# Kernel optimization log

Hardware: AMD Instinct MI355X
Metric: run time of the kernel (lower is better)

Reference implementation:

```python
import jax, jax.numpy as jnp
import numpy as np

N, C, P, K = 100000, 64, 64, 16  # points, in_planes, planes, nsample
EPS = 1e-5

def _bn(y, g, b, m, v):
    # inference-mode batchnorm over channel (last) dim
    return (y - m) * (g * jax.lax.rsqrt(v + EPS)) + b

def setup_inputs() -> dict:
    key = jax.random.key(0)
    ks = jax.random.split(key, 12)
    p = jax.random.normal(ks[0], (N, 3), jnp.float32)
    x = jax.random.normal(ks[1], (N, C), jnp.float32)
    idx = jax.random.randint(ks[2], (N, K), 0, N, jnp.int32)
    s = 0.05
    w1 = jax.random.normal(ks[3], (C, P), jnp.float32) * s
    conv_w = jax.random.normal(ks[4], (P, P + 3), jnp.float32) * s  # Conv1d(P+3, P, 1) weight squeezed
    w3 = jax.random.normal(ks[5], (P, P), jnp.float32) * s
    def bn_params(k):
        k1, k2 = jax.random.split(k)
        return (jnp.ones((P,), jnp.float32),                      # gamma
                jnp.zeros((P,), jnp.float32),                     # beta
                jax.random.normal(k1, (P,), jnp.float32) * 0.01,  # running mean
                jnp.abs(jax.random.normal(k2, (P,), jnp.float32)) * 0.1 + 1.0)  # running var
    g1, b1, m1, v1 = bn_params(ks[6])
    g2, b2, m2, v2 = bn_params(ks[7])
    g3, b3, m3, v3 = bn_params(ks[8])
    return dict(p=p, x=x, idx=idx, w1=w1, g1=g1, b1=b1, m1=m1, v1=v1,
                conv_w=conv_w, g2=g2, b2=b2, m2=m2, v2=v2,
                w3=w3, g3=g3, b3=b3, m3=m3, v3=v3)

def reference(p, x, idx, w1, g1, b1, m1, v1, conv_w, g2, b2, m2, v2, w3, g3, b3, m3, v3):
    identity = x
    h = jax.nn.relu(_bn(x @ w1, g1, b1, m1, v1))                     # [N, P]
    # queryandgroup with use_xyz=True: concat(relative xyz, neighbor feats)
    rel = p[idx] - p[:, None, :]                                      # [N, K, 3]
    grouped = jnp.concatenate([rel, h[idx]], axis=-1)                 # [N, K, 3+P]
    e = jnp.einsum('nkc,oc->nko', grouped, conv_w)                    # conv1x1 -> [N, K, P]
    e = jax.nn.relu(_bn(e, g2, b2, m2, v2))
    f = jnp.max(e, axis=1)                                            # max over neighbors -> [N, P]
    out = jax.nn.relu(_bn(f @ w3, g3, b3, m3, v3) + identity)         # [N, P]
    return out
```

## Files before the change

kernel.cpp:

```cpp
#include <hip/hip_runtime.h>
#include <stdint.h>


#define EPS 1e-5f

typedef unsigned short u16;
typedef unsigned int u32;
typedef __attribute__((ext_vector_type(8))) short bf16x8;
typedef __attribute__((ext_vector_type(4))) float f32x4;

__device__ __forceinline__ float b2f(u16 u) { return __uint_as_float(((u32)u) << 16); }
__device__ __forceinline__ u16 f2b(float f) {
    u32 u = __float_as_uint(f);
    u32 r = u + 0x7fffu + ((u >> 16) & 1u);
    return (u16)(r >> 16);
}
__device__ __forceinline__ bool is_bf16(const void* g) { return ((const u32*)g)[0] == 0x3F803F80u; }
__device__ __forceinline__ float ldval(const void* p, size_t i, bool isbf) {
    return isbf ? b2f(((const u16*)p)[i]) : ((const float*)p)[i];
}
#define MFMA16(a, b, c) __builtin_amdgcn_mfma_f32_16x16x32_bf16(a, b, c, 0, 0, 0)

__device__ __forceinline__ bf16x8 asbf(uint4 u) {
    union { uint4 u; bf16x8 b; } c;
    c.u = u;
    return c.b;
}

__device__ __forceinline__ bf16x8 ldrow8(const void* base, size_t row, int coff, bool isbf) {
    if (isbf) {
        const u16* pp = (const u16*)base + row * 64 + coff;
        return asbf(*(const uint4*)pp);
    } else {
        const float* pp = (const float*)base + row * 64 + coff;
        float4 q0 = ((const float4*)pp)[0], q1 = ((const float4*)pp)[1];
        bf16x8 r;
        r[0] = (short)f2b(q0.x); r[1] = (short)f2b(q0.y);
        r[2] = (short)f2b(q0.z); r[3] = (short)f2b(q0.w);
        r[4] = (short)f2b(q1.x); r[5] = (short)f2b(q1.y);
        r[6] = (short)f2b(q1.z); r[7] = (short)f2b(q1.w);
        return r;
    }
}

__global__ void __launch_bounds__(256)
k_prep(const void* __restrict__ w1, const void* __restrict__ cw, const void* __restrict__ w3,
       const void* __restrict__ g1, const void* __restrict__ b1, const void* __restrict__ m1,
       const void* __restrict__ v1, const void* __restrict__ g2, const void* __restrict__ b2,
       const void* __restrict__ m2, const void* __restrict__ v2, const void* __restrict__ g3,
       const void* __restrict__ b3, const void* __restrict__ m3, const void* __restrict__ v3,
       uint4* __restrict__ w1f, uint4* __restrict__ cwf, uint4* __restrict__ w3f,
       float* __restrict__ bnst) {
    const bool isbf = is_bf16(g1);
    const int tid = blockIdx.x * blockDim.x + threadIdx.x;
    if (tid < 512) {
        int f = tid >> 6, lane = tid & 63;
        int ch = f >> 2, t = f & 3, quad = lane >> 4, c0 = lane & 15;
        union { uint4 u; bf16x8 b; } r;
#pragma unroll
        for (int j = 0; j < 8; ++j) {
            int c = ch * 32 + quad * 8 + j, o = t * 16 + c0;
            r.b[j] = (short)f2b(ldval(w1, (size_t)c * 64 + o, isbf));
        }
        w1f[f * 64 + lane] = r.u;
    } else if (tid < 1280) {
        int f = (tid - 512) >> 6, lane = tid & 63;
        int ch = f >> 2, t = f & 3, quad = lane >> 4, c0 = lane & 15;
        union { uint4 u; bf16x8 b; } r;
#pragma unroll
        for (int j = 0; j < 8; ++j) {
            int o = t * 16 + c0;
            short val;
            if (ch < 2) {
                int c = ch * 32 + quad * 8 + j;
                val = (short)f2b(ldval(cw, (size_t)o * 67 + 3 + c, isbf));
            } else {
                int pc = quad * 8 + j;
                val = (pc < 3) ? (short)f2b(ldval(cw, (size_t)o * 67 + pc, isbf)) : (short)0;
            }
            r.b[j] = val;
        }
        cwf[f * 64 + lane] = r.u;
    } else if (tid < 1792) {
        int f = (tid - 1280) >> 6, lane = tid & 63;
        int ch = f >> 2, t = f & 3, quad = lane >> 4, c0 = lane & 15;
        union { uint4 u; bf16x8 b; } r;
#pragma unroll
        for (int j = 0; j < 8; ++j) {
            int c = ch * 32 + quad * 8 + j, o = t * 16 + c0;
            r.b[j] = (short)f2b(ldval(w3, (size_t)c * 64 + o, isbf));
        }
        w3f[f * 64 + lane] = r.u;
    } else if (tid < 2176) {
        int id = tid - 1792;
        int bn = id >> 7, rem = id & 127, ch = rem & 63, which = rem >> 6;
        const void* g = (bn == 0) ? g1 : (bn == 1) ? g2 : g3;
        const void* b = (bn == 0) ? b1 : (bn == 1) ? b2 : b3;
        const void* m = (bn == 0) ? m1 : (bn == 1) ? m2 : m3;
        const void* v = (bn == 0) ? v1 : (bn == 1) ? v2 : v3;
        float gv = ldval(g, ch, isbf), bv = ldval(b, ch, isbf);
        float mv = ldval(m, ch, isbf), vv = ldval(v, ch, isbf);
        float s = gv * rsqrtf(vv + EPS);
        float t = bv - mv * s;
        bnst[bn * 128 + which * 64 + ch] = which ? t : s;
    }
}

__global__ void __launch_bounds__(256, 3)
k_h_mfma(const void* __restrict__ x, const void* __restrict__ p, const void* __restrict__ g1,
         const uint4* __restrict__ w1f, const float* __restrict__ bnst,
         float4* __restrict__ p4, u16* __restrict__ hbf, int N) {
    const bool isbf = is_bf16(g1);
    const int lane = threadIdx.x & 63, quad = lane >> 4, col = lane & 15;
    const int wave = blockIdx.x * (blockDim.x >> 6) + (threadIdx.x >> 6);
    const int nw = gridDim.x * (blockDim.x >> 6);
    bf16x8 B00 = asbf(w1f[0 * 64 + lane]), B01 = asbf(w1f[1 * 64 + lane]);
    bf16x8 B02 = asbf(w1f[2 * 64 + lane]), B03 = asbf(w1f[3 * 64 + lane]);
    bf16x8 B10 = asbf(w1f[4 * 64 + lane]), B11 = asbf(w1f[5 * 64 + lane]);
    bf16x8 B12 = asbf(w1f[6 * 64 + lane]), B13 = asbf(w1f[7 * 64 + lane]);
    f32x4 sv, tv;
#pragma unroll
    for (int t = 0; t < 4; ++t) {
        sv[t] = bnst[0 * 128 + 0 + t * 16 + col];
        tv[t] = bnst[0 * 128 + 64 + t * 16 + col];
    }
    const int nt = (N + 15) >> 4;
    for (int ti = wave; ti < nt; ti += nw) {
        const int n0 = ti * 16;
        int ra = n0 + col;
        if (ra > N - 1) ra = N - 1;
        bf16x8 A0 = ldrow8(x, (size_t)ra, quad * 8, isbf);
        bf16x8 A1 = ldrow8(x, (size_t)ra, 32 + quad * 8, isbf);
        if (quad == 0 && n0 + col < N) {
            int row = n0 + col;
            float4 pv;
            pv.x = ldval(p, (size_t)row * 3 + 0, isbf);
            pv.y = ldval(p, (size_t)row * 3 + 1, isbf);
            pv.z = ldval(p, (size_t)row * 3 + 2, isbf);
            pv.w = 0.f;
            p4[row] = pv;
        }
        f32x4 acc0 = {0.f, 0.f, 0.f, 0.f}, acc1 = acc0, acc2 = acc0, acc3 = acc0;
        acc0 = MFMA16(A0, B00, acc0); acc0 = MFMA16(A1, B10, acc0);
        acc1 = MFMA16(A0, B01, acc1); acc1 = MFMA16(A1, B11, acc1);
        acc2 = MFMA16(A0, B02, acc2); acc2 = MFMA16(A1, B12, acc2);
        acc3 = MFMA16(A0, B03, acc3); acc3 = MFMA16(A1, B13, acc3);
#define STT(acc, t)                                                            \
    {                                                                          \
        _Pragma("unroll") for (int r = 0; r < 4; ++r) {                        \
            int row = n0 + quad * 4 + r;                                       \
            if (row < N) {                                                     \
                float e = acc[r] * sv[t] + tv[t];                              \
                hbf[(size_t)row * 64 + (t)*16 + col] = f2b(fmaxf(e, 0.f));     \
            }                                                                  \
        }                                                                      \
    }
        STT(acc0, 0) STT(acc1, 1) STT(acc2, 2) STT(acc3, 3)
#undef STT
    }
}

template <bool FORCE_BF16>
__global__ void __launch_bounds__(256, 3)
k_conv_mfma(const u16* __restrict__ hbf, const float4* __restrict__ p4,
            const int* __restrict__ idx, const uint4* __restrict__ cwf,
            const float* __restrict__ bnst, const void* __restrict__ g2,
            void* __restrict__ fout, int N) {
    const bool isbf = is_bf16(g2);
    const int lane = threadIdx.x & 63, quad = lane >> 4, col = lane & 15;
    const int wave = blockIdx.x * (blockDim.x >> 6) + (threadIdx.x >> 6);
    const int nw = gridDim.x * (blockDim.x >> 6);
    bf16x8 B00 = asbf(cwf[0 * 64 + lane]), B01 = asbf(cwf[1 * 64 + lane]);
    bf16x8 B02 = asbf(cwf[2 * 64 + lane]), B03 = asbf(cwf[3 * 64 + lane]);
    bf16x8 B10 = asbf(cwf[4 * 64 + lane]), B11 = asbf(cwf[5 * 64 + lane]);
    bf16x8 B12 = asbf(cwf[6 * 64 + lane]), B13 = asbf(cwf[7 * 64 + lane]);
    bf16x8 B20 = asbf(cwf[8 * 64 + lane]), B21 = asbf(cwf[9 * 64 + lane]);
    bf16x8 B22 = asbf(cwf[10 * 64 + lane]), B23 = asbf(cwf[11 * 64 + lane]);
    f32x4 sv, tv;
#pragma unroll
    for (int t = 0; t < 4; ++t) {
        sv[t] = bnst[1 * 128 + 0 + t * 16 + col];
        tv[t] = bnst[1 * 128 + 64 + t * 16 + col];
    }
    const int step = 2 * nw;
    int b = 2 * wave;
    int ja_c = 0, jb_c = 0;
    uint4 h0a_c, h1a_c, h0b_c, h1b_c;
    if (b < N) {
        const int na = b, nb = (b + 1 < N) ? b + 1 : b;
        ja_c = idx[(size_t)na * 16 + col];
        jb_c = idx[(size_t)nb * 16 + col];
        const uint4* ra = (const uint4*)(hbf + (size_t)ja_c * 64);
        const uint4* rb = (const uint4*)(hbf + (size_t)jb_c * 64);
        h0a_c = ra[quad]; h1a_c = ra[4 + quad];
        h0b_c = rb[quad]; h1b_c = rb[4 + quad];
    }
    for (; b < N; b += step) {
        const int bnext = b + step;
        int ja_n = 0, jb_n = 0;
        uint4 h0a_n = {0, 0, 0, 0}, h1a_n = h0a_n, h0b_n = h0a_n, h1b_n = h0a_n;
        if (bnext < N) {
            const int na = bnext, nb = (bnext + 1 < N) ? bnext + 1 : bnext;
            ja_n = idx[(size_t)na * 16 + col];
            jb_n = idx[(size_t)nb * 16 + col];
            const uint4* ra = (const uint4*)(hbf + (size_t)ja_n * 64);
            const uint4* rb = (const uint4*)(hbf + (size_t)jb_n * 64);
            h0a_n = ra[quad]; h1a_n = ra[4 + quad];
            h0b_n = rb[quad]; h1b_n = rb[4 + quad];
        }
        const int na = b, nb = (b + 1 < N) ? b + 1 : b;
        float4 pja = p4[ja_c], pjb = p4[jb_c];
        float4 pna = p4[na], pnb = p4[nb];
        bf16x8 A2a = {0, 0, 0, 0, 0, 0, 0, 0}, A2b = A2a;
        if (quad == 0) {
            A2a[0] = (short)f2b(pja.x - pna.x);
            A2a[1] = (short)f2b(pja.y - pna.y);
            A2a[2] = (short)f2b(pja.z - pna.z);
            A2b[0] = (short)f2b(pjb.x - pnb.x);
            A2b[1] = (short)f2b(pjb.y - pnb.y);
            A2b[2] = (short)f2b(pjb.z - pnb.z);
        }
        f32x4 z = {0.f, 0.f, 0.f, 0.f};
        f32x4 acc0a = z, acc1a = z, acc2a = z, acc3a = z;
        f32x4 acc0b = z, acc1b = z, acc2b = z, acc3b = z;
        bf16x8 a0a = asbf(h0a_c), a1a = asbf(h1a_c);
        bf16x8 a0b = asbf(h0b_c), a1b = asbf(h1b_c);
        acc0a = MFMA16(a0a, B00, acc0a); acc0b = MFMA16(a0b, B00, acc0b);
        acc1a = MFMA16(a0a, B01, acc1a); acc1b = MFMA16(a0b, B01, acc1b);
        acc2a = MFMA16(a0a, B02, acc2a); acc2b = MFMA16(a0b, B02, acc2b);
        acc3a = MFMA16(a0a, B03, acc3a); acc3b = MFMA16(a0b, B03, acc3b);
        acc0a = MFMA16(a1a, B10, acc0a); acc0b = MFMA16(a1b, B10, acc0b);
        acc1a = MFMA16(a1a, B11, acc1a); acc1b = MFMA16(a1b, B11, acc1b);
        acc2a = MFMA16(a1a, B12, acc2a); acc2b = MFMA16(a1b, B12, acc2b);
        acc3a = MFMA16(a1a, B13, acc3a); acc3b = MFMA16(a1b, B13, acc3b);
        acc0a = MFMA16(A2a, B20, acc0a); acc0b = MFMA16(A2b, B20, acc0b);
        acc1a = MFMA16(A2a, B21, acc1a); acc1b = MFMA16(A2b, B21, acc1b);
        acc2a = MFMA16(A2a, B22, acc2a); acc2b = MFMA16(A2b, B22, acc2b);
        acc3a = MFMA16(A2a, B23, acc3a); acc3b = MFMA16(A2b, B23, acc3b);
#define RED(acc, t, dst)                                                       \
    {                                                                          \
        float mx = fmaxf(fmaxf(acc[0], acc[1]), fmaxf(acc[2], acc[3]));        \
        float mn = fminf(fminf(acc[0], acc[1]), fminf(acc[2], acc[3]));        \
        mx = fmaxf(mx, __shfl_xor(mx, 16));                                    \
        mn = fminf(mn, __shfl_xor(mn, 16));                                    \
        mx = fmaxf(mx, __shfl_xor(mx, 32));                                    \
        mn = fminf(mn, __shfl_xor(mn, 32));                                    \
        float e = fmaxf(sv[t] * mx + tv[t], sv[t] * mn + tv[t]);               \
        dst = fmaxf(e, 0.f);                                                   \
    }
        {
            float f0, f1, f2, f3;
            RED(acc0a, 0, f0) RED(acc1a, 1, f1) RED(acc2a, 2, f2) RED(acc3a, 3, f3)
            float fv = (lane < 16) ? f0 : (lane < 32) ? f1 : (lane < 48) ? f2 : f3;
            if (FORCE_BF16 || isbf)
                ((u16*)fout)[(size_t)na * 64 + lane] = f2b(fv);
            else
                ((float*)fout)[(size_t)na * 64 + lane] = fv;
        }
        if (b + 1 < N) {
            float f0, f1, f2, f3;
            RED(acc0b, 0, f0) RED(acc1b, 1, f1) RED(acc2b, 2, f2) RED(acc3b, 3, f3)
            float fv = (lane < 16) ? f0 : (lane < 32) ? f1 : (lane < 48) ? f2 : f3;
            if (FORCE_BF16 || isbf)
                ((u16*)fout)[(size_t)nb * 64 + lane] = f2b(fv);
            else
                ((float*)fout)[(size_t)nb * 64 + lane] = fv;
        }
#undef RED
        ja_c = ja_n; jb_c = jb_n;
        h0a_c = h0a_n; h1a_c = h1a_n; h0b_c = h0b_n; h1b_c = h1b_n;
    }
}

template <bool FIN_BF16_ALWAYS>
__global__ void __launch_bounds__(256, 3)
k_out_mfma(const void* __restrict__ fin, const void* __restrict__ x,
           const uint4* __restrict__ w3f, const float* __restrict__ bnst,
           const void* __restrict__ g3, void* __restrict__ out, int N) {
    const bool isbf = is_bf16(g3);
    const bool finbf = FIN_BF16_ALWAYS ? true : isbf;
    const int lane = threadIdx.x & 63, quad = lane >> 4, col = lane & 15;
    const int wave = blockIdx.x * (blockDim.x >> 6) + (threadIdx.x >> 6);
    const int nw = gridDim.x * (blockDim.x >> 6);
    bf16x8 B00 = asbf(w3f[0 * 64 + lane]), B01 = asbf(w3f[1 * 64 + lane]);
    bf16x8 B02 = asbf(w3f[2 * 64 + lane]), B03 = asbf(w3f[3 * 64 + lane]);
    bf16x8 B10 = asbf(w3f[4 * 64 + lane]), B11 = asbf(w3f[5 * 64 + lane]);
    bf16x8 B12 = asbf(w3f[6 * 64 + lane]), B13 = asbf(w3f[7 * 64 + lane]);
    f32x4 sv, tv;
#pragma unroll
    for (int t = 0; t < 4; ++t) {
        sv[t] = bnst[2 * 128 + 0 + t * 16 + col];
        tv[t] = bnst[2 * 128 + 64 + t * 16 + col];
    }
    const int nt = (N + 15) >> 4;
    for (int ti = wave; ti < nt; ti += nw) {
        const int n0 = ti * 16;
        int ra = n0 + col;
        if (ra > N - 1) ra = N - 1;
        bf16x8 A0 = ldrow8(fin, (size_t)ra, quad * 8, finbf);
        bf16x8 A1 = ldrow8(fin, (size_t)ra, 32 + quad * 8, finbf);
        f32x4 acc0 = {0.f, 0.f, 0.f, 0.f}, acc1 = acc0, acc2 = acc0, acc3 = acc0;
        acc0 = MFMA16(A0, B00, acc0); acc0 = MFMA16(A1, B10, acc0);
        acc1 = MFMA16(A0, B01, acc1); acc1 = MFMA16(A1, B11, acc1);
        acc2 = MFMA16(A0, B02, acc2); acc2 = MFMA16(A1, B12, acc2);
        acc3 = MFMA16(A0, B03, acc3); acc3 = MFMA16(A1, B13, acc3);
#define STT(acc, t)                                                            \
    {                                                                          \
        _Pragma("unroll") for (int r = 0; r < 4; ++r) {                        \
            int row = n0 + quad * 4 + r;                                       \
            if (row < N) {                                                     \
                int o_ = (t)*16 + col;                                         \
                float e = acc[r] * sv[t] + tv[t] +                             \
                          ldval(x, (size_t)row * 64 + o_, isbf);               \
                e = fmaxf(e, 0.f);                                             \
                if (isbf)                                                      \
                    ((u16*)out)[(size_t)row * 64 + o_] = f2b(e);               \
                else                                                           \
                    ((float*)out)[(size_t)row * 64 + o_] = e;                  \
            }                                                                  \
        }                                                                      \
    }
        STT(acc0, 0) STT(acc1, 1) STT(acc2, 2) STT(acc3, 3)
#undef STT
    }
}

__device__ __forceinline__ void load_col64(const void* w, int lane, bool isbf, float* col) {
#pragma unroll
    for (int c = 0; c < 64; ++c) col[c] = ldval(w, (size_t)c * 64 + lane, isbf);
}
__device__ __forceinline__ float dot64(const void* x, size_t off, bool isbf, const float* col) {
    float a0 = 0.f;
#pragma unroll
    for (int c = 0; c < 64; ++c) a0 += ldval(x, off + c, isbf) * col[c];
    return a0;
}
__device__ __forceinline__ void bn_st(const void* g, const void* b, const void* m,
                                      const void* v, int o, bool isbf, float& s, float& t) {
    float gv = ldval(g, o, isbf), bv = ldval(b, o, isbf);
    float mv = ldval(m, o, isbf), vv = ldval(v, o, isbf);
    s = gv * rsqrtf(vv + EPS);
    t = bv - mv * s;
}
__global__ void __launch_bounds__(256) k_mono(const void* __restrict__ p, const void* __restrict__ x,
                                              const int* __restrict__ idx, const void* __restrict__ w1,
                                              const void* __restrict__ g1, const void* __restrict__ b1,
                                              const void* __restrict__ m1, const void* __restrict__ v1,
                                              const void* __restrict__ cw, const void* __restrict__ g2,
                                              const void* __restrict__ b2, const void* __restrict__ m2,
                                              const void* __restrict__ v2, const void* __restrict__ w3,
                                              const void* __restrict__ g3, const void* __restrict__ b3,
                                              const void* __restrict__ m3, const void* __restrict__ v3,
                                              void* __restrict__ out, int N) {
    const bool isbf = is_bf16(g1);
    const int lane = threadIdx.x & 63;
    const int wave = blockIdx.x * (blockDim.x >> 6) + (threadIdx.x >> 6);
    const int nw = gridDim.x * (blockDim.x >> 6);
    float w1col[64];
    load_col64(w1, lane, isbf, w1col);
    float w3col[64];
    load_col64(w3, lane, isbf, w3col);
    float s1, t1, s2, t2, s3, t3;
    bn_st(g1, b1, m1, v1, lane, isbf, s1, t1);
    bn_st(g2, b2, m2, v2, lane, isbf, s2, t2);
    bn_st(g3, b3, m3, v3, lane, isbf, s3, t3);
    for (int n = wave; n < N; n += nw) {
        const int4* ir = (const int4*)(idx + (size_t)n * 16);
        float pnx = ldval(p, (size_t)n * 3 + 0, isbf);
        float pny = ldval(p, (size_t)n * 3 + 1, isbf);
        float pnz = ldval(p, (size_t)n * 3 + 2, isbf);
        float fmx = 0.f;
        for (int kk = 0; kk < 4; ++kk) {
            const int4 iv = ir[kk];
#pragma unroll
            for (int t = 0; t < 4; ++t) {
                const int j = (t == 0) ? iv.x : (t == 1) ? iv.y : (t == 2) ? iv.z : iv.w;
                float hr = dot64(x, (size_t)j * 64, isbf, w1col);
                float hv = fmaxf(hr * s1 + t1, 0.f);
                float a0 = (ldval(p, (size_t)j * 3 + 0, isbf) - pnx) * ldval(cw, (size_t)lane * 67 + 0, isbf) +
                           (ldval(p, (size_t)j * 3 + 1, isbf) - pny) * ldval(cw, (size_t)lane * 67 + 1, isbf) +
                           (ldval(p, (size_t)j * 3 + 2, isbf) - pnz) * ldval(cw, (size_t)lane * 67 + 2, isbf);
#pragma unroll
                for (int c = 0; c < 64; ++c)
                    a0 += __shfl(hv, c) * ldval(cw, (size_t)lane * 67 + 3 + c, isbf);
                fmx = fmaxf(fmx, a0 * s2 + t2);
            }
        }
        float a = 0.f;
#pragma unroll
        for (int c = 0; c < 64; ++c) a += __shfl(fmx, c) * w3col[c];
        float r = a * s3 + t3 + ldval(x, (size_t)n * 64 + lane, isbf);
        r = fmaxf(r, 0.f);
        if (isbf)
            ((u16*)out)[(size_t)n * 64 + lane] = f2b(r);
        else
            ((float*)out)[(size_t)n * 64 + lane] = r;
    }
}

extern "C" void kernel_launch(void* const* d_in, const int* in_sizes, int n_in,
                              void* d_out, int out_size, void* d_ws, size_t ws_size,
                              hipStream_t stream) {
    const void* p = d_in[0];
    const void* x = d_in[1];
    const int* idx = (const int*)d_in[2];
    const void* w1 = d_in[3];
    const void* g1 = d_in[4];
    const void* b1 = d_in[5];
    const void* m1 = d_in[6];
    const void* v1 = d_in[7];
    const void* cw = d_in[8];
    const void* g2 = d_in[9];
    const void* b2 = d_in[10];
    const void* m2 = d_in[11];
    const void* v2 = d_in[12];
    const void* w3 = d_in[13];
    const void* g3 = d_in[14];
    const void* b3 = d_in[15];
    const void* m3 = d_in[16];
    const void* v3 = d_in[17];
    const int N = in_sizes[0] / 3;

    const int blk = 256;
    const int nt = (N + 15) >> 4;
    int gh = (nt + 3) >> 2;
    if (gh < 1) gh = 1;
    const int gc = 768;

    const size_t hb = (size_t)N * 64 * sizeof(u16);
    const size_t p4b = (size_t)N * sizeof(float4);
    const size_t packb = 8192 + 12288 + 8192 + 1536;
    const size_t need_hf = 256 + 2 * hb + p4b + packb;
    const size_t need_h = 256 + hb + p4b + packb;

    if (ws_size >= need_h) {
        char* base = (char*)d_ws + 256;
        const bool big = (ws_size >= need_hf);
        u16* h = (u16*)base;
        u16* f = big ? (u16*)(base + hb) : nullptr;
        char* rest = base + (big ? 2 * hb : hb);
        float4* p4 = (float4*)rest;
        uint4* w1f = (uint4*)(rest + p4b);
        uint4* cwf = (uint4*)(rest + p4b + 8192);
        uint4* w3f = (uint4*)(rest + p4b + 8192 + 12288);
        float* bnst = (float*)(rest + p4b + 8192 + 12288 + 8192);
        k_prep<<<9, blk, 0, stream>>>(w1, cw, w3, g1, b1, m1, v1, g2, b2, m2, v2,
                                      g3, b3, m3, v3, w1f, cwf, w3f, bnst);
        k_h_mfma<<<gh, blk, 0, stream>>>(x, p, g1, w1f, bnst, p4, h, N);
        if (big) {
            k_conv_mfma<true><<<gc, blk, 0, stream>>>(h, p4, idx, cwf, bnst, g2, (void*)f, N);
            k_out_mfma<true><<<gh, blk, 0, stream>>>((const void*)f, x, w3f, bnst, g3, d_out, N);
        } else {
            k_conv_mfma<false><<<gc, blk, 0, stream>>>(h, p4, idx, cwf, bnst, g2, d_out, N);
            k_out_mfma<false><<<gh, blk, 0, stream>>>((const void*)d_out, x, w3f, bnst, g3, d_out, N);
        }
    } else {
        k_mono<<<2048, blk, 0, stream>>>(p, x, idx, w1, g1, b1, m1, v1, cw, g2, b2, m2, v2,
                                         w3, g3, b3, m3, v3, d_out, N);
    }
}
```

Baseline: 181.5 us.

## Fuse all stages into one cooperative kernel with grid-wide syncs

Refactors the prep, h, conv and output stages into device-function bodies and runs them in a single persistent cooperative kernel, separated by grid.sync() barriers. The aim is to remove the launch gaps and tail drain between the four separate kernel launches. If the cooperative launch fails, the code falls back to the original multi-kernel path. In exchange, every stage now runs with the conv grid size and the register budget of the fused kernel, and the grid barriers have their own cost.

```diff
diff --git a/kernel.cpp b/kernel.cpp
--- a/kernel.cpp
+++ b/kernel.cpp
@@ -1,5 +1,8 @@
 #include <hip/hip_runtime.h>
+#include <hip/hip_cooperative_groups.h>
 #include <stdint.h>
+
+namespace cg = cooperative_groups;
 
 
 #define EPS 1e-5f
@@ -43,16 +46,14 @@
     }
 }
 
-__global__ void __launch_bounds__(256)
-k_prep(const void* __restrict__ w1, const void* __restrict__ cw, const void* __restrict__ w3,
-       const void* __restrict__ g1, const void* __restrict__ b1, const void* __restrict__ m1,
-       const void* __restrict__ v1, const void* __restrict__ g2, const void* __restrict__ b2,
-       const void* __restrict__ m2, const void* __restrict__ v2, const void* __restrict__ g3,
-       const void* __restrict__ b3, const void* __restrict__ m3, const void* __restrict__ v3,
-       uint4* __restrict__ w1f, uint4* __restrict__ cwf, uint4* __restrict__ w3f,
-       float* __restrict__ bnst) {
-    const bool isbf = is_bf16(g1);
-    const int tid = blockIdx.x * blockDim.x + threadIdx.x;
+
+__device__ __forceinline__ void prep_body(
+    int tid, bool isbf,
+    const void* w1, const void* cw, const void* w3,
+    const void* g1, const void* b1, const void* m1, const void* v1,
+    const void* g2, const void* b2, const void* m2, const void* v2,
+    const void* g3, const void* b3, const void* m3, const void* v3,
+    uint4* w1f, uint4* cwf, uint4* w3f, float* bnst) {
     if (tid < 512) {
         int f = tid >> 6, lane = tid & 63;
         int ch = f >> 2, t = f & 3, quad = lane >> 4, c0 = lane & 15;
@@ -106,14 +107,10 @@
     }
 }
 
-__global__ void __launch_bounds__(256, 3)
-k_h_mfma(const void* __restrict__ x, const void* __restrict__ p, const void* __restrict__ g1,
-         const uint4* __restrict__ w1f, const float* __restrict__ bnst,
-         float4* __restrict__ p4, u16* __restrict__ hbf, int N) {
-    const bool isbf = is_bf16(g1);
-    const int lane = threadIdx.x & 63, quad = lane >> 4, col = lane & 15;
-    const int wave = blockIdx.x * (blockDim.x >> 6) + (threadIdx.x >> 6);
-    const int nw = gridDim.x * (blockDim.x >> 6);
+__device__ __forceinline__ void h_body(
+    int wave, int nw, int lane, int quad, int col, bool isbf,
+    const void* x, const void* p, const uint4* w1f, const float* bnst,
+    float4* p4, u16* hbf, int N) {
     bf16x8 B00 = asbf(w1f[0 * 64 + lane]), B01 = asbf(w1f[1 * 64 + lane]);
     bf16x8 B02 = asbf(w1f[2 * 64 + lane]), B03 = asbf(w1f[3 * 64 + lane]);
     bf16x8 B10 = asbf(w1f[4 * 64 + lane]), B11 = asbf(w1f[5 * 64 + lane]);
@@ -121,8 +118,8 @@
     f32x4 sv, tv;
 #pragma unroll
     for (int t = 0; t < 4; ++t) {
-        sv[t] = bnst[0 * 128 + 0 + t * 16 + col];
-        tv[t] = bnst[0 * 128 + 64 + t * 16 + col];
+        sv[t] = bnst[0 + t * 16 + col];
+        tv[t] = bnst[64 + t * 16 + col];
     }
     const int nt = (N + 15) >> 4;
     for (int ti = wave; ti < nt; ti += nw) {
@@ -161,15 +158,10 @@
 }
 
 template <bool FORCE_BF16>
-__global__ void __launch_bounds__(256, 3)
-k_conv_mfma(const u16* __restrict__ hbf, const float4* __restrict__ p4,
-            const int* __restrict__ idx, const uint4* __restrict__ cwf,
-            const float* __restrict__ bnst, const void* __restrict__ g2,
-            void* __restrict__ fout, int N) {
-    const bool isbf = is_bf16(g2);
-    const int lane = threadIdx.x & 63, quad = lane >> 4, col = lane & 15;
-    const int wave = blockIdx.x * (blockDim.x >> 6) + (threadIdx.x >> 6);
-    const int nw = gridDim.x * (blockDim.x >> 6);
+__device__ __forceinline__ void conv_body(
+    int wave, int nw, int lane, int quad, int col, bool isbf,
+    const u16* hbf, const float4* p4, const int* idx,
+    const uint4* cwf, const float* bnst, void* fout, int N) {
     bf16x8 B00 = asbf(cwf[0 * 64 + lane]), B01 = asbf(cwf[1 * 64 + lane]);
     bf16x8 B02 = asbf(cwf[2 * 64 + lane]), B03 = asbf(cwf[3 * 64 + lane]);
     bf16x8 B10 = asbf(cwf[4 * 64 + lane]), B11 = asbf(cwf[5 * 64 + lane]);
@@ -179,13 +171,13 @@
     f32x4 sv, tv;
 #pragma unroll
     for (int t = 0; t < 4; ++t) {
-        sv[t] = bnst[1 * 128 + 0 + t * 16 + col];
-        tv[t] = bnst[1 * 128 + 64 + t * 16 + col];
+        sv[t] = bnst[128 + 0 + t * 16 + col];
+        tv[t] = bnst[128 + 64 + t * 16 + col];
     }
     const int step = 2 * nw;
     int b = 2 * wave;
     int ja_c = 0, jb_c = 0;
-    uint4 h0a_c, h1a_c, h0b_c, h1b_c;
+    uint4 h0a_c = {0, 0, 0, 0}, h1a_c = h0a_c, h0b_c = h0a_c, h1b_c = h0a_c;
     if (b < N) {
         const int na = b, nb = (b + 1 < N) ? b + 1 : b;
         ja_c = idx[(size_t)na * 16 + col];
@@ -273,15 +265,11 @@
 }
 
 template <bool FIN_BF16_ALWAYS>
-__global__ void __launch_bounds__(256, 3)
-k_out_mfma(const void* __restrict__ fin, const void* __restrict__ x,
-           const uint4* __restrict__ w3f, const float* __restrict__ bnst,
-           const void* __restrict__ g3, void* __restrict__ out, int N) {
-    const bool isbf = is_bf16(g3);
+__device__ __forceinline__ void out_body(
+    int wave, int nw, int lane, int quad, int col, bool isbf,
+    const void* fin, const void* x, const uint4* w3f, const float* bnst,
+    void* out, int N) {
     const bool finbf = FIN_BF16_ALWAYS ? true : isbf;
-    const int lane = threadIdx.x & 63, quad = lane >> 4, col = lane & 15;
-    const int wave = blockIdx.x * (blockDim.x >> 6) + (threadIdx.x >> 6);
-    const int nw = gridDim.x * (blockDim.x >> 6);
     bf16x8 B00 = asbf(w3f[0 * 64 + lane]), B01 = asbf(w3f[1 * 64 + lane]);
     bf16x8 B02 = asbf(w3f[2 * 64 + lane]), B03 = asbf(w3f[3 * 64 + lane]);
     bf16x8 B10 = asbf(w3f[4 * 64 + lane]), B11 = asbf(w3f[5 * 64 + lane]);
@@ -289,8 +277,8 @@
     f32x4 sv, tv;
 #pragma unroll
     for (int t = 0; t < 4; ++t) {
-        sv[t] = bnst[2 * 128 + 0 + t * 16 + col];
-        tv[t] = bnst[2 * 128 + 64 + t * 16 + col];
+        sv[t] = bnst[256 + 0 + t * 16 + col];
+        tv[t] = bnst[256 + 64 + t * 16 + col];
     }
     const int nt = (N + 15) >> 4;
     for (int ti = wave; ti < nt; ti += nw) {
@@ -323,6 +311,87 @@
         STT(acc0, 0) STT(acc1, 1) STT(acc2, 2) STT(acc3, 3)
 #undef STT
     }
+}
+
+template <bool BIG>
+__global__ void __launch_bounds__(256, 3)
+k_all(const void* p, const void* x, const int* idx,
+      const void* w1, const void* cw, const void* w3,
+      const void* g1, const void* b1, const void* m1, const void* v1,
+      const void* g2, const void* b2, const void* m2, const void* v2,
+      const void* g3, const void* b3, const void* m3, const void* v3,
+      u16* hbf, float4* p4, u16* fws,
+      uint4* w1f, uint4* cwf, uint4* w3f, float* bnst,
+      void* out, int N) {
+    cg::grid_group grid = cg::this_grid();
+    const bool isbf = is_bf16(g1);
+    const int lane = threadIdx.x & 63, quad = lane >> 4, col = lane & 15;
+    const int wave = blockIdx.x * (blockDim.x >> 6) + (threadIdx.x >> 6);
+    const int nw = gridDim.x * (blockDim.x >> 6);
+    const int tid = blockIdx.x * blockDim.x + threadIdx.x;
+
+    prep_body(tid, isbf, w1, cw, w3, g1, b1, m1, v1, g2, b2, m2, v2,
+              g3, b3, m3, v3, w1f, cwf, w3f, bnst);
+    grid.sync();
+    h_body(wave, nw, lane, quad, col, isbf, x, p, w1f, bnst, p4, hbf, N);
+    grid.sync();
+    if (BIG)
+        conv_body<true>(wave, nw, lane, quad, col, isbf, hbf, p4, idx, cwf, bnst, (void*)fws, N);
+    else
+        conv_body<false>(wave, nw, lane, quad, col, isbf, hbf, p4, idx, cwf, bnst, out, N);
+    grid.sync();
+    if (BIG)
+        out_body<true>(wave, nw, lane, quad, col, isbf, (const void*)fws, x, w3f, bnst, out, N);
+    else
+        out_body<false>(wave, nw, lane, quad, col, isbf, (const void*)out, x, w3f, bnst, out, N);
+}
+
+__global__ void __launch_bounds__(256)
+k_prep(const void* w1, const void* cw, const void* w3,
+       const void* g1, const void* b1, const void* m1, const void* v1,
+       const void* g2, const void* b2, const void* m2, const void* v2,
+       const void* g3, const void* b3, const void* m3, const void* v3,
+       uint4* w1f, uint4* cwf, uint4* w3f, float* bnst) {
+    const bool isbf = is_bf16(g1);
+    const int tid = blockIdx.x * blockDim.x + threadIdx.x;
+    prep_body(tid, isbf, w1, cw, w3, g1, b1, m1, v1, g2, b2, m2, v2,
+              g3, b3, m3, v3, w1f, cwf, w3f, bnst);
+}
+
+__global__ void __launch_bounds__(256, 3)
+k_h_mfma(const void* __restrict__ x, const void* __restrict__ p, const void* __restrict__ g1,
+         const uint4* __restrict__ w1f, const float* __restrict__ bnst,
+         float4* __restrict__ p4, u16* __restrict__ hbf, int N) {
+    const bool isbf = is_bf16(g1);
+    const int lane = threadIdx.x & 63, quad = lane >> 4, col = lane & 15;
+    const int wave = blockIdx.x * (blockDim.x >> 6) + (threadIdx.x >> 6);
+    const int nw = gridDim.x * (blockDim.x >> 6);
+    h_body(wave, nw, lane, quad, col, isbf, x, p, w1f, bnst, p4, hbf, N);
+}
+
+template <bool FORCE_BF16>
+__global__ void __launch_bounds__(256, 3)
+k_conv_mfma(const u16* __restrict__ hbf, const float4* __restrict__ p4,
+            const int* __restrict__ idx, const uint4* __restrict__ cwf,
+            const float* __restrict__ bnst, const void* __restrict__ g2,
+            void* __restrict__ fout, int N) {
+    const bool isbf = is_bf16(g2);
+    const int lane = threadIdx.x & 63, quad = lane >> 4, col = lane & 15;
+    const int wave = blockIdx.x * (blockDim.x >> 6) + (threadIdx.x >> 6);
+    const int nw = gridDim.x * (blockDim.x >> 6);
+    conv_body<FORCE_BF16>(wave, nw, lane, quad, col, isbf, hbf, p4, idx, cwf, bnst, fout, N);
+}
+
+template <bool FIN_BF16_ALWAYS>
+__global__ void __launch_bounds__(256, 3)
+k_out_mfma(const void* __restrict__ fin, const void* __restrict__ x,
+           const uint4* __restrict__ w3f, const float* __restrict__ bnst,
+           const void* __restrict__ g3, void* __restrict__ out, int N) {
+    const bool isbf = is_bf16(g3);
+    const int lane = threadIdx.x & 63, quad = lane >> 4, col = lane & 15;
+    const int wave = blockIdx.x * (blockDim.x >> 6) + (threadIdx.x >> 6);
+    const int nw = gridDim.x * (blockDim.x >> 6);
+    out_body<FIN_BF16_ALWAYS>(wave, nw, lane, quad, col, isbf, fin, x, w3f, bnst, out, N);
 }
 
 __device__ __forceinline__ void load_col64(const void* w, int lane, bool isbf, float* col) {
@@ -444,6 +513,24 @@
         uint4* cwf = (uint4*)(rest + p4b + 8192);
         uint4* w3f = (uint4*)(rest + p4b + 8192 + 12288);
         float* bnst = (float*)(rest + p4b + 8192 + 12288 + 8192);
+
+        int Nv = N;
+        void* outv = d_out;
+        void* args[] = {(void*)&p,  (void*)&x,  (void*)&idx, (void*)&w1, (void*)&cw,
+                        (void*)&w3, (void*)&g1, (void*)&b1,  (void*)&m1, (void*)&v1,
+                        (void*)&g2, (void*)&b2, (void*)&m2,  (void*)&v2, (void*)&g3,
+                        (void*)&b3, (void*)&m3, (void*)&v3,  (void*)&h,  (void*)&p4,
+                        (void*)&f,  (void*)&w1f, (void*)&cwf, (void*)&w3f, (void*)&bnst,
+                        (void*)&outv, (void*)&Nv};
+        hipError_t err;
+        if (big)
+            err = hipLaunchCooperativeKernel((void*)k_all<true>, dim3(gc), dim3(blk),
+                                             args, 0, stream);
+        else
+            err = hipLaunchCooperativeKernel((void*)k_all<false>, dim3(gc), dim3(blk),
+                                             args, 0, stream);
+        if (err == hipSuccess) return;
+
         k_prep<<<9, blk, 0, stream>>>(w1, cw, w3, g1, b1, m1, v1, g2, b2, m2, v2,
                                       g3, b3, m3, v3, w1f, cwf, w3f, bnst);
         k_h_mfma<<<gh, blk, 0, stream>>>(x, p, g1, w1f, bnst, p4, h, N);
```

After: 462.2 us. +154.7%, slower.
